# Performance work log

Hardware: AMD Instinct MI355X
Metric: run time of the kernel (lower is better)

Reference implementation:

```python
import jax, jax.numpy as jnp
import numpy as np

N = 20000      # nodes
E = 160000     # edges (before self loops)
IN = 128       # in_channels (== edge_dim)
H = 8          # heads
C = 64         # out_channels per head
NEG_SLOPE = 0.2


def setup_inputs() -> dict:
    key = jax.random.key(0)
    ks = jax.random.split(key, 8)
    s_in = np.float32(1.0 / np.sqrt(IN))
    s_att = np.float32(1.0 / np.sqrt(C))
    return {
        "x": jax.random.normal(ks[0], (N, IN), jnp.float32),
        "edge_index": jax.random.randint(ks[1], (2, E), 0, N, dtype=jnp.int32),
        "edge_attr": jax.random.normal(ks[2], (E, IN), jnp.float32),
        "Wl": jax.random.normal(ks[3], (IN, H * C), jnp.float32) * s_in,
        "Wr": jax.random.normal(ks[4], (IN, H * C), jnp.float32) * s_in,
        "We": jax.random.normal(ks[5], (IN, H * C), jnp.float32) * s_in,
        "att": jax.random.normal(ks[6], (H, C), jnp.float32) * s_att,
        "bias": jnp.zeros((H * C,), jnp.float32),
    }


def reference(x, edge_index, edge_attr, Wl, Wr, We, att, bias):
    n = x.shape[0]
    e = edge_attr.shape[0]
    src, dst = edge_index[0], edge_index[1]

    # add self loops; self-loop edge_attr = per-target-node mean of incoming
    # edge attrs (PyG fill_value='mean'); nodes with no in-edges get zeros.
    cnt = jax.ops.segment_sum(jnp.ones((e,), x.dtype), dst, num_segments=n)
    loop_attr = jax.ops.segment_sum(edge_attr, dst, num_segments=n) / jnp.maximum(cnt, 1.0)[:, None]
    loops = jnp.arange(n, dtype=src.dtype)
    src_f = jnp.concatenate([src, loops])          # [E+N]
    dst_f = jnp.concatenate([dst, loops])          # [E+N]
    ea = jnp.concatenate([edge_attr, loop_attr], axis=0)  # [E+N, IN]

    xl = (x @ Wl).reshape(n, H, C)   # source projection
    xr = (x @ Wr).reshape(n, H, C)   # target projection
    xe = (ea @ We).reshape(-1, H, C)  # edge projection

    # GATv2 score: att . LeakyReLU(xl_j + xr_i + xe)
    m = jax.nn.leaky_relu(xl[src_f] + xr[dst_f] + xe, NEG_SLOPE)  # [E+N, H, C]
    logits = jnp.einsum('ehc,hc->eh', m, att)                      # [E+N, H]

    # segment softmax over incoming edges of each target node
    lmax = jax.ops.segment_max(logits, dst_f, num_segments=n)      # [N, H]
    p = jnp.exp(logits - lmax[dst_f])
    denom = jax.ops.segment_sum(p, dst_f, num_segments=n)
    alpha = p / denom[dst_f]                                       # [E+N, H]

    # weighted scatter-add aggregation of source features
    out = jax.ops.segment_sum(alpha[:, :, None] * xl[src_f], dst_f, num_segments=n)
    return out.reshape(n, H * C) + bias
```

## Files before the change

kernel.cpp:

```cpp
#include <hip/hip_runtime.h>

#define N_NODES 20000
#define E_EDGES 160000
#define IN_CH 128
#define H_HEADS 8
#define C_CH 64
#define HC 512
#define M_TOT (E_EDGES + N_NODES)
#define NEG_SLOPE 0.2f
#define NCHUNK ((N_NODES + 255) / 256)

typedef __attribute__((ext_vector_type(8))) short bf16x8;
typedef __attribute__((ext_vector_type(4))) float f32x4;

__device__ __forceinline__ unsigned short f2bf(float f) {
    unsigned u = __float_as_uint(f);
    unsigned r = (u + 0x7FFFu + ((u >> 16) & 1u)) >> 16;
    return (unsigned short)r;
}
__device__ __forceinline__ float bf2f(unsigned short s) {
    return __uint_as_float((unsigned)s << 16);
}
__device__ __forceinline__ float bfx(const bf16x8& v0, const bf16x8& v1, int idx) {
    return bf2f((unsigned short)((idx < 8) ? v0[idx] : v1[idx - 8]));
}

__global__ void k_deg(const int* __restrict__ ei, int* __restrict__ deg) {
    int e = blockIdx.x * blockDim.x + threadIdx.x;
    if (e >= E_EDGES) return;
    atomicAdd(&deg[ei[E_EDGES + e]], 1);
}

__global__ void k_scan1(const int* __restrict__ deg, int* __restrict__ bsum) {
    __shared__ int red[256];
    int tid = threadIdx.x;
    int i = blockIdx.x * 256 + tid;
    red[tid] = (i < N_NODES) ? deg[i] + 1 : 0;
    __syncthreads();
    for (int off = 128; off > 0; off >>= 1) {
        if (tid < off) red[tid] += red[tid + off];
        __syncthreads();
    }
    if (tid == 0) bsum[blockIdx.x] = red[0];
}

__global__ void k_scan2(const int* __restrict__ bsum, int* __restrict__ boff) {
    if (threadIdx.x == 0) {
        int run = 0;
        for (int b = 0; b < NCHUNK; ++b) { boff[b] = run; run += bsum[b]; }
    }
}

__global__ void k_scan3(const int* __restrict__ deg, const int* __restrict__ boff,
                        int* __restrict__ rowptr, int* __restrict__ cursor,
                        int* __restrict__ eidx, int* __restrict__ src_s,
                        int* __restrict__ dst_s) {
    __shared__ int buf[256];
    int tid = threadIdx.x;
    int i = blockIdx.x * 256 + tid;
    int v = (i < N_NODES) ? deg[i] + 1 : 0;
    buf[tid] = v;
    __syncthreads();
    for (int off = 1; off < 256; off <<= 1) {
        int tv = (tid >= off) ? buf[tid - off] : 0;
        __syncthreads();
        buf[tid] += tv;
        __syncthreads();
    }
    if (i < N_NODES) {
        int excl = boff[blockIdx.x] + buf[tid] - v;
        rowptr[i] = excl;
        eidx[excl] = E_EDGES + i;
        src_s[excl] = i;
        dst_s[excl] = i;
        cursor[i] = excl + 1;
        if (i == N_NODES - 1) rowptr[N_NODES] = excl + v;
    }
}

__global__ void k_fill(const int* __restrict__ ei, int* __restrict__ cursor,
                       int* __restrict__ eidx, int* __restrict__ src_s,
                       int* __restrict__ dst_s) {
    int e = blockIdx.x * blockDim.x + threadIdx.x;
    if (e >= E_EDGES) return;
    int d = ei[E_EDGES + e];
    int slot = atomicAdd(&cursor[d], 1);
    eidx[slot] = e;
    src_s[slot] = ei[e];
    dst_s[slot] = d;
}

__global__ void k_loop_attr(const int* __restrict__ rowptr, const int* __restrict__ eidx,
                            const float* __restrict__ ea, float* __restrict__ loop_attr) {
    int wave = (blockIdx.x * blockDim.x + threadIdx.x) >> 6;
    int lane = threadIdx.x & 63;
    if (wave >= N_NODES) return;
    int beg = rowptr[wave] + 1, end = rowptr[wave + 1];
    int cnt = end - beg;
    float s0 = 0.f, s1 = 0.f;
    if (beg < end) {
        const float* p_nxt = ea + (size_t)eidx[beg] * 128 + lane;
        for (int p = beg; p < end; ++p) {
            const float* cur = p_nxt;
            if (p + 1 < end) p_nxt = ea + (size_t)eidx[p + 1] * 128 + lane;
            s0 += cur[0];
            s1 += cur[64];
        }
    }
    float inv = 1.f / fmaxf((float)cnt, 1.f);
    loop_attr[(size_t)wave * 128 + lane] = s0 * inv;
    loop_attr[(size_t)wave * 128 + 64 + lane] = s1 * inv;
}

__global__ void k_trans3(const float* __restrict__ Wl, const float* __restrict__ Wr,
                         const float* __restrict__ We,
                         unsigned short* __restrict__ WlT, unsigned short* __restrict__ WrT,
                         unsigned short* __restrict__ WeT) {
    int idx = blockIdx.x * blockDim.x + threadIdx.x;
    if (idx >= HC * IN_CH) return;
    int m = blockIdx.y;
    const float* W = (m == 0) ? Wl : (m == 1) ? Wr : We;
    unsigned short* WT = (m == 0) ? WlT : (m == 1) ? WrT : WeT;
    int n = idx >> 7, k = idx & 127;
    WT[idx] = f2bf(W[(size_t)k * HC + n]);
}

__global__ void k_gemm2(const float* __restrict__ A,
                        const unsigned short* __restrict__ WlT,
                        const unsigned short* __restrict__ WrT,
                        unsigned short* __restrict__ xlb, unsigned short* __restrict__ xrb,
                        int M) {
    __shared__ short As[64 * 128];
    int row0 = blockIdx.x * 64;
    int sel = blockIdx.y >> 1;
    const unsigned short* BT = sel ? WrT : WlT;
    unsigned short* Cb = sel ? xrb : xlb;
    int t = threadIdx.x;
    {
        int row = t >> 2, c0 = (t & 3) * 32;
        int gr = row0 + row;
        int sw = (row & 7) << 4;
        const float* src = A + (size_t)gr * 128 + c0;
        #pragma unroll
        for (int i = 0; i < 4; ++i) {
            bf16x8 v;
            if (gr < M) {
                const float4* p = (const float4*)(src + i * 8);
                float4 f0 = p[0], f1 = p[1];
                v[0] = f2bf(f0.x); v[1] = f2bf(f0.y); v[2] = f2bf(f0.z); v[3] = f2bf(f0.w);
                v[4] = f2bf(f1.x); v[5] = f2bf(f1.y); v[6] = f2bf(f1.z); v[7] = f2bf(f1.w);
            } else {
                #pragma unroll
                for (int j = 0; j < 8; ++j) v[j] = 0;
            }
            int off = row * 256 + (((c0 + i * 8) * 2) ^ sw);
            *(bf16x8*)((char*)As + off) = v;
        }
    }
    __syncthreads();

    int w = t >> 6, l = t & 63;
    int lr = l & 15, lk = l >> 4;
    int col0 = (blockIdx.y & 1) * 256 + w * 64;

    f32x4 acc[4][4];
    #pragma unroll
    for (int mi = 0; mi < 4; ++mi)
        #pragma unroll
        for (int fj = 0; fj < 4; ++fj)
            #pragma unroll
            for (int q = 0; q < 4; ++q) acc[mi][fj][q] = 0.f;

    #pragma unroll
    for (int k0 = 0; k0 < 4; ++k0) {
        bf16x8 a4[4];
        #pragma unroll
        for (int mi = 0; mi < 4; ++mi) {
            int row = mi * 16 + lr;
            int off = row * 256 + ((k0 * 64 + lk * 16) ^ ((row & 7) << 4));
            a4[mi] = *(const bf16x8*)((const char*)As + off);
        }
        #pragma unroll
        for (int fj = 0; fj < 4; ++fj) {
            bf16x8 b = *(const bf16x8*)(BT + (size_t)(col0 + fj * 16 + lr) * 128 + k0 * 32 + lk * 8);
            #pragma unroll
            for (int mi = 0; mi < 4; ++mi)
                acc[mi][fj] = __builtin_amdgcn_mfma_f32_16x16x32_bf16(a4[mi], b, acc[mi][fj], 0, 0, 0);
        }
    }
    #pragma unroll
    for (int mi = 0; mi < 4; ++mi) {
        #pragma unroll
        for (int reg = 0; reg < 4; ++reg) {
            int r = row0 + mi * 16 + lk * 4 + reg;
            if (r < M) {
                unsigned short* cp = Cb + (size_t)r * 512 + col0 + lr;
                #pragma unroll
                for (int fj = 0; fj < 4; ++fj) cp[fj * 16] = f2bf(acc[mi][fj][reg]);
            }
        }
    }
}

#define PREF(R, CB, SLOT) { \
    int s_ = s_src[R], d_ = s_dst[R]; \
    const bf16x8* xp_ = (const bf16x8*)(xlb + (size_t)s_ * 512 + (CB) + q * 16); \
    pa0[SLOT] = xp_[0]; pa1[SLOT] = xp_[1]; \
    const bf16x8* rp_ = (const bf16x8*)(xrb + (size_t)d_ * 512 + (CB) + q * 16); \
    pb0[SLOT] = rp_[0]; pb1[SLOT] = rp_[1]; }

__global__ void k_fused(const int* __restrict__ eidx, const int* __restrict__ src_s,
                        const int* __restrict__ dst_s, const int* __restrict__ rowptr,
                        const float* __restrict__ ea, const float* __restrict__ loop_attr,
                        const unsigned short* __restrict__ WeT,
                        const unsigned short* __restrict__ xlb,
                        const unsigned short* __restrict__ xrb,
                        const float* __restrict__ att, const float* __restrict__ bias,
                        float* __restrict__ logits, float* __restrict__ out) {
    __shared__ short As[64 * 128];
    __shared__ float xeT[4][16][68];
    __shared__ float att_s[512];
    __shared__ float lg[64][8];
    __shared__ int s_src[64], s_dst[64];
    __shared__ int own_node[64], own_beg[64], own_len[64];
    __shared__ int n_own;
    int row0 = blockIdx.x * 64;
    int t = threadIdx.x;

    if (t == 0) n_own = 0;
    __syncthreads();

    if (t < 64) {
        int p = row0 + t;
        int s = 0, d = 0;
        if (p < M_TOT) {
            s = src_s[p]; d = dst_s[p];
            int pb = rowptr[d], pe = rowptr[d + 1];
            if (pb == p && pe <= row0 + 64) {
                int idx = atomicAdd(&n_own, 1);
                own_node[idx] = d; own_beg[idx] = t; own_len[idx] = pe - pb;
            }
        }
        s_src[t] = s; s_dst[t] = d;
    }
    att_s[t] = att[t];
    att_s[t + 256] = att[t + 256];
    {
        int row = t >> 2, c0 = (t & 3) * 32;
        int p = row0 + row;
        int sw = (row & 7) << 4;
        const float* src = nullptr;
        if (p < M_TOT) {
            int e = eidx[p];
            src = (e < E_EDGES) ? ea + (size_t)e * 128 + c0
                                : loop_attr + (size_t)(e - E_EDGES) * 128 + c0;
        }
        #pragma unroll
        for (int i = 0; i < 4; ++i) {
            bf16x8 v;
            if (src) {
                const float4* p4 = (const float4*)(src + i * 8);
                float4 f0 = p4[0], f1 = p4[1];
                v[0] = f2bf(f0.x); v[1] = f2bf(f0.y); v[2] = f2bf(f0.z); v[3] = f2bf(f0.w);
                v[4] = f2bf(f1.x); v[5] = f2bf(f1.y); v[6] = f2bf(f1.z); v[7] = f2bf(f1.w);
            } else {
                #pragma unroll
                for (int j = 0; j < 8; ++j) v[j] = 0;
            }
            int off = row * 256 + (((c0 + i * 8) * 2) ^ sw);
            *(bf16x8*)((char*)As + off) = v;
        }
    }
    __syncthreads();

    int w = t >> 6, l = t & 63;
    int lr = l & 15, lk = l >> 4;
    int eloc = l >> 2, q = l & 3;
    int cb0 = w * 128;

    bf16x8 pa0[2], pa1[2], pb0[2], pb1[2];
    f32x4 acc[4][4];

    PREF(eloc, cb0, 0);

    #pragma unroll
    for (int hh = 0; hh < 2; ++hh) {
        int cb = cb0 + hh * 64;
        int h = w * 2 + hh;

        #pragma unroll
        for (int mi = 0; mi < 4; ++mi)
            #pragma unroll
            for (int fj = 0; fj < 4; ++fj)
                #pragma unroll
                for (int qq = 0; qq < 4; ++qq) acc[mi][fj][qq] = 0.f;

        #pragma unroll
        for (int k0 = 0; k0 < 4; ++k0) {
            bf16x8 a4[4];
            #pragma unroll
            for (int mi = 0; mi < 4; ++mi) {
                int row = mi * 16 + lr;
                int off = row * 256 + ((k0 * 64 + lk * 16) ^ ((row & 7) << 4));
                a4[mi] = *(const bf16x8*)((const char*)As + off);
            }
            #pragma unroll
            for (int fj = 0; fj < 4; ++fj) {
                bf16x8 b = *(const bf16x8*)(WeT + (size_t)(cb + fj * 16 + lr) * 128 + k0 * 32 + lk * 8);
                #pragma unroll
                for (int mi = 0; mi < 4; ++mi)
                    acc[mi][fj] = __builtin_amdgcn_mfma_f32_16x16x32_bf16(a4[mi], b, acc[mi][fj], 0, 0, 0);
            }
        }

        #pragma unroll
        for (int mi = 0; mi < 4; ++mi) {
            if (mi < 3) { PREF(mi * 16 + 16 + eloc, cb, (mi + 1) & 1); }
            else if (hh == 0) { PREF(eloc, cb + 64, 0); }

            #pragma unroll
            for (int fj = 0; fj < 4; ++fj)
                #pragma unroll
                for (int reg = 0; reg < 4; ++reg)
                    xeT[w][lk * 4 + reg][fj * 16 + lr] = acc[mi][fj][reg];

            const bf16x8 ca0 = pa0[mi & 1], ca1 = pa1[mi & 1];
            const bf16x8 cb0v = pb0[mi & 1], cb1v = pb1[mi & 1];

            float sum = 0.f;
            #pragma unroll
            for (int sg = 0; sg < 4; ++sg) {
                float4 xe4 = *(const float4*)&xeT[w][eloc][q * 16 + sg * 4];
                float4 av  = *(const float4*)&att_s[cb + q * 16 + sg * 4];
                float v0 = xe4.x + bfx(ca0, ca1, sg * 4 + 0) + bfx(cb0v, cb1v, sg * 4 + 0);
                float v1 = xe4.y + bfx(ca0, ca1, sg * 4 + 1) + bfx(cb0v, cb1v, sg * 4 + 1);
                float v2 = xe4.z + bfx(ca0, ca1, sg * 4 + 2) + bfx(cb0v, cb1v, sg * 4 + 2);
                float v3 = xe4.w + bfx(ca0, ca1, sg * 4 + 3) + bfx(cb0v, cb1v, sg * 4 + 3);
                v0 = (v0 > 0.f) ? v0 : v0 * NEG_SLOPE;
                v1 = (v1 > 0.f) ? v1 : v1 * NEG_SLOPE;
                v2 = (v2 > 0.f) ? v2 : v2 * NEG_SLOPE;
                v3 = (v3 > 0.f) ? v3 : v3 * NEG_SLOPE;
                sum = fmaf(av.x, v0, sum);
                sum = fmaf(av.y, v1, sum);
                sum = fmaf(av.z, v2, sum);
                sum = fmaf(av.w, v3, sum);
            }
            sum += __shfl_xor(sum, 1, 64);
            sum += __shfl_xor(sum, 2, 64);
            if (q == 0) {
                int rloc = mi * 16 + eloc;
                lg[rloc][h] = sum;
                int p = row0 + rloc;
                if (p < M_TOT) logits[(size_t)p * 8 + h] = sum;
            }
        }
    }
    __syncthreads();

    {
        int lane = t & 63;
        int h = lane >> 3;
        for (int o = w; o < n_own; o += 4) {
            int d = own_node[o], rb = own_beg[o], len = own_len[o];
            float m = -3.4e38f;
            for (int j = 0; j < len; ++j) m = fmaxf(m, lg[rb + j][h]);
            float den = 0.f;
            for (int j = 0; j < len; ++j) den += __expf(lg[rb + j][h] - m);
            float rden = 1.f / den;
            float ac[8] = {};
            bf16x8 v_nxt = *(const bf16x8*)(xlb + (size_t)s_src[rb] * 512 + lane * 8);
            for (int j = 0; j < len; ++j) {
                bf16x8 v = v_nxt;
                if (j + 1 < len)
                    v_nxt = *(const bf16x8*)(xlb + (size_t)s_src[rb + j + 1] * 512 + lane * 8);
                float alpha = __expf(lg[rb + j][h] - m) * rden;
                #pragma unroll
                for (int jj = 0; jj < 8; ++jj) ac[jj] = fmaf(alpha, bf2f((unsigned short)v[jj]), ac[jj]);
            }
            float4* op = (float4*)(out + (size_t)d * 512 + lane * 8);
            const float4* bp = (const float4*)(bias + lane * 8);
            float4 bv0 = bp[0], bv1 = bp[1];
            float4 r0 = { ac[0] + bv0.x, ac[1] + bv0.y, ac[2] + bv0.z, ac[3] + bv0.w };
            float4 r1 = { ac[4] + bv1.x, ac[5] + bv1.y, ac[6] + bv1.z, ac[7] + bv1.w };
            op[0] = r0; op[1] = r1;
        }
    }
}

__global__ void k_cleanup(const int* __restrict__ rowptr, const int* __restrict__ src_s,
                          const float* __restrict__ logits,
                          const unsigned short* __restrict__ xlb, const float* __restrict__ bias,
                          float* __restrict__ out) {
    int node = (blockIdx.x * blockDim.x + threadIdx.x) >> 6;
    int lane = threadIdx.x & 63;
    if (node >= N_NODES) return;
    int beg = rowptr[node], end = rowptr[node + 1];
    if ((beg >> 6) == ((end - 1) >> 6)) return;
    int h = lane >> 3;

    float m = -3.4e38f;
    for (int p = beg; p < end; ++p) m = fmaxf(m, logits[(size_t)p * 8 + h]);
    float den = 0.f;
    for (int p = beg; p < end; ++p) den += __expf(logits[(size_t)p * 8 + h] - m);
    float rden = 1.f / den;

    float acc[8] = {};
    bf16x8 v_nxt = *(const bf16x8*)(xlb + (size_t)src_s[beg] * 512 + lane * 8);
    for (int p = beg; p < end; ++p) {
        bf16x8 v = v_nxt;
        float lgv = logits[(size_t)p * 8 + h];
        if (p + 1 < end)
            v_nxt = *(const bf16x8*)(xlb + (size_t)src_s[p + 1] * 512 + lane * 8);
        float alpha = __expf(lgv - m) * rden;
        #pragma unroll
        for (int j = 0; j < 8; ++j) acc[j] = fmaf(alpha, bf2f((unsigned short)v[j]), acc[j]);
    }
    float4* op = (float4*)(out + (size_t)node * 512 + lane * 8);
    const float4* bp = (const float4*)(bias + lane * 8);
    float4 bv0 = bp[0], bv1 = bp[1];
    float4 r0 = { acc[0] + bv0.x, acc[1] + bv0.y, acc[2] + bv0.z, acc[3] + bv0.w };
    float4 r1 = { acc[4] + bv1.x, acc[5] + bv1.y, acc[6] + bv1.z, acc[7] + bv1.w };
    op[0] = r0; op[1] = r1;
}

extern "C" void kernel_launch(void* const* d_in, const int* in_sizes, int n_in,
                              void* d_out, int out_size, void* d_ws, size_t ws_size,
                              hipStream_t stream) {
    const float* x    = (const float*)d_in[0];
    const int*   ei   = (const int*)d_in[1];
    const float* ea   = (const float*)d_in[2];
    const float* Wl   = (const float*)d_in[3];
    const float* Wr   = (const float*)d_in[4];
    const float* We   = (const float*)d_in[5];
    const float* att  = (const float*)d_in[6];
    const float* bias = (const float*)d_in[7];
    float* out = (float*)d_out;

    unsigned short* xlb = (unsigned short*)d_ws;
    unsigned short* xrb = xlb + (size_t)N_NODES * HC;
    unsigned short* WlT = xrb + (size_t)N_NODES * HC;
    unsigned short* WrT = WlT + HC * IN_CH;
    unsigned short* WeT = WrT + HC * IN_CH;
    float* loop_attr = (float*)(WeT + HC * IN_CH);
    float* logits    = loop_attr + (size_t)N_NODES * IN_CH;
    int* deg         = (int*)(logits + (size_t)M_TOT * 8);
    int* rowptr      = deg + N_NODES;
    int* cursor      = rowptr + N_NODES + 1;
    int* eidx        = cursor + N_NODES;
    int* src_s       = eidx + M_TOT;
    int* dst_s       = src_s + M_TOT;
    int* bsum        = dst_s + M_TOT;
    int* boff        = bsum + NCHUNK;

    const int B = 256;
    hipMemsetAsync(deg, 0, N_NODES * sizeof(int), stream);
    k_deg<<<(E_EDGES + B - 1) / B, B, 0, stream>>>(ei, deg);
    k_scan1<<<NCHUNK, B, 0, stream>>>(deg, bsum);
    k_scan2<<<1, 64, 0, stream>>>(bsum, boff);
    k_scan3<<<NCHUNK, B, 0, stream>>>(deg, boff, rowptr, cursor, eidx, src_s, dst_s);
    k_fill<<<(E_EDGES + B - 1) / B, B, 0, stream>>>(ei, cursor, eidx, src_s, dst_s);
    k_loop_attr<<<(N_NODES * 64 + B - 1) / B, B, 0, stream>>>(rowptr, eidx, ea, loop_attr);
    k_trans3<<<dim3((HC * IN_CH + B - 1) / B, 3), B, 0, stream>>>(Wl, Wr, We, WlT, WrT, WeT);
    k_gemm2<<<dim3((N_NODES + 63) / 64, 4), B, 0, stream>>>(x, WlT, WrT, xlb, xrb, N_NODES);
    k_fused<<<(M_TOT + 63) / 64, B, 0, stream>>>(eidx, src_s, dst_s, rowptr, ea, loop_attr,
                                                 WeT, xlb, xrb, att, bias, logits, out);
    k_cleanup<<<((size_t)N_NODES * 64 + B - 1) / B, B, 0, stream>>>(rowptr, src_s, logits,
                                                                    xlb, bias, out);
}
```

Measured before the change: 257.2 us.

## Pre-sort edge attrs into CSR-ordered bf16 buffer and load via global_load_lds

The loop-attr kernel now also writes every edge attribute as bf16 into a CSR-ordered buffer, with the self-loop mean stored at each node's first slot. The fused kernel then streams contiguous bf16 rows straight into LDS with direct global-to-LDS loads and a pre-swizzled chunk index. This removes the gathered fp32 loads, per-element conversions and register staging from the fused kernel. In exchange, the prep kernel writes an extra bf16 copy of all edge attributes, and the fused kernel now depends on an explicit vmcnt wait.

```diff
diff --git a/kernel.cpp b/kernel.cpp
--- a/kernel.cpp
+++ b/kernel.cpp
@@ -24,6 +24,10 @@
 __device__ __forceinline__ float bfx(const bf16x8& v0, const bf16x8& v1, int idx) {
     return bf2f((unsigned short)((idx < 8) ? v0[idx] : v1[idx - 8]));
 }
+
+#define GLOAD_LDS16(gsrc, ldst) \
+    __builtin_amdgcn_global_load_lds((const __attribute__((address_space(1))) void*)(gsrc), \
+                                     (__attribute__((address_space(3))) void*)(ldst), 16, 0, 0)
 
 __global__ void k_deg(const int* __restrict__ ei, int* __restrict__ deg) {
     int e = blockIdx.x * blockDim.x + threadIdx.x;
@@ -90,26 +94,28 @@
     dst_s[slot] = d;
 }
 
-__global__ void k_loop_attr(const int* __restrict__ rowptr, const int* __restrict__ eidx,
-                            const float* __restrict__ ea, float* __restrict__ loop_attr) {
-    int wave = (blockIdx.x * blockDim.x + threadIdx.x) >> 6;
+__global__ void k_prep(const int* __restrict__ rowptr, const int* __restrict__ eidx,
+                       const float* __restrict__ ea, unsigned short* __restrict__ eab) {
+    int node = (blockIdx.x * blockDim.x + threadIdx.x) >> 6;
     int lane = threadIdx.x & 63;
-    if (wave >= N_NODES) return;
-    int beg = rowptr[wave] + 1, end = rowptr[wave + 1];
-    int cnt = end - beg;
+    if (node >= N_NODES) return;
+    int beg = rowptr[node], end = rowptr[node + 1];
+    int cnt = end - beg - 1;
     float s0 = 0.f, s1 = 0.f;
-    if (beg < end) {
-        const float* p_nxt = ea + (size_t)eidx[beg] * 128 + lane;
-        for (int p = beg; p < end; ++p) {
+    if (beg + 1 < end) {
+        const float* p_nxt = ea + (size_t)eidx[beg + 1] * 128 + lane;
+        for (int p = beg + 1; p < end; ++p) {
             const float* cur = p_nxt;
             if (p + 1 < end) p_nxt = ea + (size_t)eidx[p + 1] * 128 + lane;
-            s0 += cur[0];
-            s1 += cur[64];
+            float v0 = cur[0], v1 = cur[64];
+            s0 += v0; s1 += v1;
+            eab[(size_t)p * 128 + lane] = f2bf(v0);
+            eab[(size_t)p * 128 + 64 + lane] = f2bf(v1);
         }
     }
     float inv = 1.f / fmaxf((float)cnt, 1.f);
-    loop_attr[(size_t)wave * 128 + lane] = s0 * inv;
-    loop_attr[(size_t)wave * 128 + 64 + lane] = s1 * inv;
+    eab[(size_t)beg * 128 + lane] = f2bf(s0 * inv);
+    eab[(size_t)beg * 128 + 64 + lane] = f2bf(s1 * inv);
 }
 
 __global__ void k_trans3(const float* __restrict__ Wl, const float* __restrict__ Wr,
@@ -209,9 +215,9 @@
     const bf16x8* rp_ = (const bf16x8*)(xrb + (size_t)d_ * 512 + (CB) + q * 16); \
     pb0[SLOT] = rp_[0]; pb1[SLOT] = rp_[1]; }
 
-__global__ void k_fused(const int* __restrict__ eidx, const int* __restrict__ src_s,
-                        const int* __restrict__ dst_s, const int* __restrict__ rowptr,
-                        const float* __restrict__ ea, const float* __restrict__ loop_attr,
+__global__ void k_fused(const int* __restrict__ src_s, const int* __restrict__ dst_s,
+                        const int* __restrict__ rowptr,
+                        const unsigned short* __restrict__ eab,
                         const unsigned short* __restrict__ WeT,
                         const unsigned short* __restrict__ xlb,
                         const unsigned short* __restrict__ xrb,
@@ -230,6 +236,22 @@
     if (t == 0) n_own = 0;
     __syncthreads();
 
+    {
+        int l = t & 63;
+        int c_base = (t >> 6) * 4;
+        #pragma unroll
+        for (int i = 0; i < 4; ++i) {
+            int c = c_base + i;
+            int row_local = c * 4 + (l >> 4);
+            int grow = row0 + row_local;
+            if (grow > M_TOT - 1) grow = M_TOT - 1;
+            int chunk = (l & 15) ^ (row_local & 7);
+            const char* src = (const char*)eab + (size_t)grow * 256 + chunk * 16;
+            char* dst = (char*)As + c * 1024;
+            GLOAD_LDS16(src, dst);
+        }
+    }
+
     if (t < 64) {
         int p = row0 + t;
         int s = 0, d = 0;
@@ -245,32 +267,8 @@
     }
     att_s[t] = att[t];
     att_s[t + 256] = att[t + 256];
-    {
-        int row = t >> 2, c0 = (t & 3) * 32;
-        int p = row0 + row;
-        int sw = (row & 7) << 4;
-        const float* src = nullptr;
-        if (p < M_TOT) {
-            int e = eidx[p];
-            src = (e < E_EDGES) ? ea + (size_t)e * 128 + c0
-                                : loop_attr + (size_t)(e - E_EDGES) * 128 + c0;
-        }
-        #pragma unroll
-        for (int i = 0; i < 4; ++i) {
-            bf16x8 v;
-            if (src) {
-                const float4* p4 = (const float4*)(src + i * 8);
-                float4 f0 = p4[0], f1 = p4[1];
-                v[0] = f2bf(f0.x); v[1] = f2bf(f0.y); v[2] = f2bf(f0.z); v[3] = f2bf(f0.w);
-                v[4] = f2bf(f1.x); v[5] = f2bf(f1.y); v[6] = f2bf(f1.z); v[7] = f2bf(f1.w);
-            } else {
-                #pragma unroll
-                for (int j = 0; j < 8; ++j) v[j] = 0;
-            }
-            int off = row * 256 + (((c0 + i * 8) * 2) ^ sw);
-            *(bf16x8*)((char*)As + off) = v;
-        }
-    }
+
+    asm volatile("s_waitcnt vmcnt(0)");
     __syncthreads();
 
     int w = t >> 6, l = t & 63;
@@ -441,8 +439,8 @@
     unsigned short* WlT = xrb + (size_t)N_NODES * HC;
     unsigned short* WrT = WlT + HC * IN_CH;
     unsigned short* WeT = WrT + HC * IN_CH;
-    float* loop_attr = (float*)(WeT + HC * IN_CH);
-    float* logits    = loop_attr + (size_t)N_NODES * IN_CH;
+    unsigned short* eab = WeT + HC * IN_CH;
+    float* logits    = (float*)(eab + (size_t)M_TOT * IN_CH);
     int* deg         = (int*)(logits + (size_t)M_TOT * 8);
     int* rowptr      = deg + N_NODES;
     int* cursor      = rowptr + N_NODES + 1;
@@ -459,11 +457,11 @@
     k_scan2<<<1, 64, 0, stream>>>(bsum, boff);
     k_scan3<<<NCHUNK, B, 0, stream>>>(deg, boff, rowptr, cursor, eidx, src_s, dst_s);
     k_fill<<<(E_EDGES + B - 1) / B, B, 0, stream>>>(ei, cursor, eidx, src_s, dst_s);
-    k_loop_attr<<<(N_NODES * 64 + B - 1) / B, B, 0, stream>>>(rowptr, eidx, ea, loop_attr);
+    k_prep<<<(N_NODES * 64 + B - 1) / B, B, 0, stream>>>(rowptr, eidx, ea, eab);
     k_trans3<<<dim3((HC * IN_CH + B - 1) / B, 3), B, 0, stream>>>(Wl, Wr, We, WlT, WrT, WeT);
     k_gemm2<<<dim3((N_NODES + 63) / 64, 4), B, 0, stream>>>(x, WlT, WrT, xlb, xrb, N_NODES);
-    k_fused<<<(M_TOT + 63) / 64, B, 0, stream>>>(eidx, src_s, dst_s, rowptr, ea, loop_attr,
-                                                 WeT, xlb, xrb, att, bias, logits, out);
+    k_fused<<<(M_TOT + 63) / 64, B, 0, stream>>>(src_s, dst_s, rowptr, eab, WeT,
+                                                 xlb, xrb, att, bias, logits, out);
     k_cleanup<<<((size_t)N_NODES * 64 + B - 1) / B, B, 0, stream>>>(rowptr, src_s, logits,
                                                                     xlb, bias, out);
 }
```

Result: slower. 262.8 us (+2.2%).
